# Kernel optimization log

Measured on AMD Instinct MI355X. Metric: run time of the kernel, lower is better.

The kernel has to match this reference:

```python
import jax, jax.numpy as jnp
import numpy as np

DEPTH = 16
Q_DIM = 64
V_DIM = 64
BATCH = 2048


def setup_inputs() -> dict:
    key = jax.random.key(0)
    k1, k2, k3 = jax.random.split(key, 3)
    query = jax.random.normal(k1, (BATCH, Q_DIM), dtype=jnp.float32)
    # internal-node keys: (2^depth - 1) nodes, each with 2 child keys of dim q_dim
    tree_key = jax.random.normal(k2, (2 ** DEPTH - 1, 2, Q_DIM), dtype=jnp.float32)
    # leaf values: 2^depth leaves of dim v_dim
    tree_value = jax.random.normal(k3, (2 ** DEPTH, V_DIM), dtype=jnp.float32)
    return {"query": query, "tree_key": tree_key, "tree_value": tree_value}


def _tree_attention(query, tree_key, tree_value, depth):
    # Hierarchical softmax attention over a complete binary tree.
    # At each internal node, a 2-way softmax over <query, child_key> logits
    # splits probability mass between left/right subtrees; leaf weight is the
    # product of probabilities along its root-to-leaf path.
    B = query.shape[0]
    probs = jnp.ones((B, 1), dtype=query.dtype)
    start = 0
    for d in range(depth):
        n = 2 ** d  # nodes at this level, stored contiguously at [start, start+n)
        level_keys = tree_key[start:start + n]           # (n, 2, q_dim)
        logits = jnp.einsum('bq,ncq->bnc', query, level_keys)  # (B, n, 2)
        p = jax.nn.softmax(logits, axis=-1)               # (B, n, 2)
        probs = (probs[:, :, None] * p).reshape(B, 2 * n)  # (B, 2n)
        start += n
    # weighted combination of leaf values: (B, 2^depth) @ (2^depth, v_dim)
    return probs @ tree_value


def reference(query, tree_key, tree_value):
    return _tree_attention(query, tree_key, tree_value, DEPTH)
```

## Files before the change

### kernel.cpp

```cpp
#include <hip/hip_runtime.h>

#define LOG2E 1.44269504088896f

typedef _Float16 half8  __attribute__((ext_vector_type(8)));
typedef _Float16 half4v __attribute__((ext_vector_type(4)));
typedef float    floatx4 __attribute__((ext_vector_type(4)));

#define WS_KD   0u
#define WS_VT   8388608u
#define WS_PART 16777216u

__device__ __forceinline__ floatx4 mfma16(half8 a, half8 b, floatx4 c) {
    return __builtin_amdgcn_mfma_f32_16x16x32_f16(a, b, c, 0, 0, 0);
}

__device__ __forceinline__ float sigmf(float d) {
    return __builtin_amdgcn_rcpf(1.0f + __builtin_amdgcn_exp2f(d * (-LOG2E)));
}

__device__ __forceinline__ void wave_lds_fence() {
    asm volatile("s_waitcnt lgkmcnt(0)" ::: "memory");
    __builtin_amdgcn_sched_barrier(0);
}

__global__ __launch_bounds__(256)
void k_prep(const float* __restrict__ tkey, const float* __restrict__ tval,
            char* __restrict__ ws)
{
    __shared__ _Float16 sT[64 * 72];
    const int bid = blockIdx.x, tid = threadIdx.x;

    {
        const int l = tid >> 2, part = tid & 3;
        const floatx4* vp = (const floatx4*)(tval + ((size_t)bid * 64 + l) * 64) + part * 4;
        #pragma unroll
        for (int t4 = 0; t4 < 4; ++t4) {
            floatx4 f = vp[t4];
            #pragma unroll
            for (int e = 0; e < 4; ++e)
                sT[(part * 16 + t4 * 4 + e) * 72 + l] = (_Float16)f[e];
        }
    }
    __syncthreads();
    {
        const int v = tid >> 2, q4 = tid & 3;
        half8 x0 = *(const half8*)(sT + v * 72 + 16 * q4);
        half8 x1 = *(const half8*)(sT + v * 72 + 16 * q4 + 8);
        char* base = ws + WS_VT + (size_t)bid * 8192;
        const int nt = v >> 4, lmv = v & 15;
        const int u0 = 2 * q4, u1 = 2 * q4 + 1;
        *(half8*)(base + (nt * 2 + (u0 >> 2)) * 1024 + (((u0 & 3) << 4) | lmv) * 16) = x0;
        *(half8*)(base + (nt * 2 + (u1 >> 2)) * 1024 + (((u1 & 3) << 4) | lmv) * 16) = x1;
    }

    #pragma unroll
    for (int k = 0; k < 2; ++k) {
        const int gt  = bid * 512 + k * 256 + tid;
        const int rid = gt >> 3, part = gt & 7;
        const int s = rid >> 6, j = rid & 63;
        const size_t dst = (size_t)WS_KD + (size_t)s * 8192
                         + ((j >> 4) * 2 + (part >> 2)) * 1024
                         + (((part & 3) << 4) | (j & 15)) * 16;
        half8 out;
        if (j < 63) {
            const int u = j + 1;
            const int f = 31 - __builtin_clz(u);
            const int i = u - (1 << f);
            const int gidx = ((1 << (10 + f)) - 1) + (s << f) + i;
            const floatx4* kp = (const floatx4*)(tkey + (size_t)gidx * 128) + part * 2;
            floatx4 a0 = kp[0], a1 = kp[1];
            floatx4 b0 = kp[16], b1 = kp[17];
            #pragma unroll
            for (int e = 0; e < 4; ++e) {
                out[e]     = (_Float16)(a0[e] - b0[e]);
                out[4 + e] = (_Float16)(a1[e] - b1[e]);
            }
        } else {
            #pragma unroll
            for (int e = 0; e < 8; ++e) out[e] = (_Float16)0.f;
        }
        *(half8*)(ws + dst) = out;
    }
}

__global__ __launch_bounds__(256, 2)
void k_main(const float* __restrict__ q,
            const float* __restrict__ tkey,
            const char* __restrict__ wsc,
            _Float16* __restrict__ pout)
{
    __shared__ _Float16 sW[4 * 64 * 72];

    const int tid  = threadIdx.x;
    const int w    = tid >> 6;
    const int lane = tid & 63;
    const int lm   = lane & 15;
    const int quad = lane >> 4;
    const int xcd  = blockIdx.x & 7;
    const int ix   = blockIdx.x >> 3;
    const int g    = xcd * 8 + (ix >> 3);
    const int tb   = ix & 7;

    _Float16* R = sW + w * (64 * 72);

    half8 qA[4][2];
    #pragma unroll
    for (int m = 0; m < 4; ++m)
        #pragma unroll
        for (int kt = 0; kt < 2; ++kt) {
            const int row = tb * 256 + 64 * w + 16 * m + lm;
            const floatx4* qp = (const floatx4*)(q + (size_t)row * 64 + kt * 32 + quad * 8);
            floatx4 f0 = qp[0], f1 = qp[1];
            half8 hv;
            #pragma unroll
            for (int e = 0; e < 4; ++e) { hv[e] = (_Float16)f0[e]; hv[4 + e] = (_Float16)f1[e]; }
            qA[m][kt] = hv;
        }

    half8 pbf[2][2];
    #pragma unroll
    for (int nt = 0; nt < 2; ++nt) {
        const int j = 16 * nt + lm;
        int gidx = -1;
        if (j < 6) {
            gidx = (1 << j) - 1 + (g >> (6 - j));
        } else if (j < 21) {
            const int u = j - 5;
            const int e = 31 - __builtin_clz(u);
            const int i = u - (1 << e);
            gidx = ((1 << (6 + e)) - 1) + (g << e) + i;
        }
        #pragma unroll
        for (int kt = 0; kt < 2; ++kt) {
            half8 out;
            if (gidx >= 0) {
                const floatx4* kp = (const floatx4*)(tkey + (size_t)gidx * 128 + kt * 32 + quad * 8);
                floatx4 a0 = kp[0], a1 = kp[1];
                floatx4 b0 = kp[16], b1 = kp[17];
                #pragma unroll
                for (int e = 0; e < 4; ++e) {
                    out[e]     = (_Float16)(a0[e] - b0[e]);
                    out[4 + e] = (_Float16)(a1[e] - b1[e]);
                }
            } else {
                #pragma unroll
                for (int e = 0; e < 8; ++e) out[e] = (_Float16)0.f;
            }
            pbf[nt][kt] = out;
        }
    }

    #pragma unroll
    for (int nt = 0; nt < 2; ++nt) {
        floatx4 acc[4];
        #pragma unroll
        for (int m = 0; m < 4; ++m) {
            acc[m][0] = 0.f; acc[m][1] = 0.f; acc[m][2] = 0.f; acc[m][3] = 0.f;
            acc[m] = mfma16(pbf[nt][0], qA[m][0], acc[m]);
            acc[m] = mfma16(pbf[nt][1], qA[m][1], acc[m]);
        }
        #pragma unroll
        for (int m = 0; m < 4; ++m) {
            half4v ph;
            #pragma unroll
            for (int r = 0; r < 4; ++r) ph[r] = (_Float16)sigmf(acc[m][r]);
            *(half4v*)(R + (16 * m + lm) * 72 + 16 * nt + 4 * quad) = ph;
        }
    }
    wave_lds_fence();

    float pref = 1.f;
    #pragma unroll
    for (int d = 0; d < 6; ++d) {
        float pv = (float)R[lane * 72 + d];
        pref *= ((g >> (5 - d)) & 1) ? (1.f - pv) : pv;
    }
    const float p6    = (float)R[lane * 72 + 6];
    const float p7_0  = (float)R[lane * 72 + 7],  p7_1  = (float)R[lane * 72 + 8];
    const float p9_0  = (float)R[lane * 72 + 9],  p9_1  = (float)R[lane * 72 + 10];
    const float p9_2  = (float)R[lane * 72 + 11], p9_3  = (float)R[lane * 72 + 12];
    const float p13_0 = (float)R[lane * 72 + 13], p13_1 = (float)R[lane * 72 + 14];
    const float p13_2 = (float)R[lane * 72 + 15], p13_3 = (float)R[lane * 72 + 16];
    const float p13_4 = (float)R[lane * 72 + 17], p13_5 = (float)R[lane * 72 + 18];
    const float p13_6 = (float)R[lane * 72 + 19], p13_7 = (float)R[lane * 72 + 20];
    wave_lds_fence();

    floatx4 O[4][4];
    #pragma unroll
    for (int m = 0; m < 4; ++m)
        #pragma unroll
        for (int nt = 0; nt < 4; ++nt) { O[m][nt][0]=0.f; O[m][nt][1]=0.f; O[m][nt][2]=0.f; O[m][nt][3]=0.f; }

    for (int sl = 0; sl < 16; ++sl) {
        const int s = (g << 4) + sl;

        const char* kdp = wsc + WS_KD + (size_t)s * 8192;
        const char* vtp = wsc + WS_VT + (size_t)s * 8192;
        half8 bfr[4][2], vf[4][2];
        #pragma unroll
        for (int nt = 0; nt < 4; ++nt)
            #pragma unroll
            for (int kt = 0; kt < 2; ++kt) {
                bfr[nt][kt] = *(const half8*)(kdp + (nt * 2 + kt) * 1024 + lane * 16);
                vf[nt][kt]  = *(const half8*)(vtp + (nt * 2 + kt) * 1024 + lane * 16);
            }

        __builtin_amdgcn_s_setprio(1);
        #pragma unroll
        for (int nt = 0; nt < 4; ++nt) {
            floatx4 acc[4];
            #pragma unroll
            for (int m = 0; m < 4; ++m) {
                acc[m][0] = 0.f; acc[m][1] = 0.f; acc[m][2] = 0.f; acc[m][3] = 0.f;
                acc[m] = mfma16(bfr[nt][0], qA[m][0], acc[m]);
                acc[m] = mfma16(bfr[nt][1], qA[m][1], acc[m]);
            }
            #pragma unroll
            for (int m = 0; m < 4; ++m) {
                half4v ph;
                #pragma unroll
                for (int r = 0; r < 4; ++r) ph[r] = (_Float16)sigmf(acc[m][r]);
                *(half4v*)(R + (16 * m + lm) * 72 + 16 * nt + 4 * quad) = ph;
            }
        }
        __builtin_amdgcn_s_setprio(0);
        wave_lds_fence();

        const int a0 = sl >> 3, a1 = sl >> 2, a2 = sl >> 1;
        float P0v = pref * (a0 ? (1.f - p6) : p6);
        { float v7 = a0 ? p7_1 : p7_0;                    P0v *= (a1 & 1) ? (1.f - v7) : v7; }
        { float v9 = (a1 == 0) ? p9_0 : (a1 == 1) ? p9_1 : (a1 == 2) ? p9_2 : p9_3;
                                                          P0v *= (a2 & 1) ? (1.f - v9) : v9; }
        { float vd = (a2 == 0) ? p13_0 : (a2 == 1) ? p13_1 : (a2 == 2) ? p13_2 : (a2 == 3) ? p13_3
                   : (a2 == 4) ? p13_4 : (a2 == 5) ? p13_5 : (a2 == 6) ? p13_6 : p13_7;
                                                          P0v *= (sl & 1) ? (1.f - vd) : vd; }

        half8 pr[8];
        #pragma unroll
        for (int t = 0; t < 8; ++t)
            pr[t] = *(const half8*)(R + lane * 72 + t * 8);
        #define PN(n) ((float)pr[(n) >> 3][(n) & 7])

        #pragma unroll
        for (int qq = 0; qq < 4; ++qq) {
            float p0 = PN(0);
            float p1 = PN(1 + (qq >> 1));
            float P2 = P0v * (((qq >> 1) & 1) ? (1.f - p0) : p0)
                           * ((qq & 1) ? (1.f - p1) : p1);
            float p2 = PN(3 + qq);
            float A3[2]; A3[0] = P2 * p2; A3[1] = P2 * (1.f - p2);
            float A4[4];
            #pragma unroll
            for (int c = 0; c < 2; ++c) {
                float pv = PN(7 + 2 * qq + c);
                A4[2 * c] = A3[c] * pv; A4[2 * c + 1] = A3[c] * (1.f - pv);
            }
            float A5[8];
            #pragma unroll
            for (int n = 0; n < 4; ++n) {
                float pv = PN(15 + 4 * qq + n);
                A5[2 * n] = A4[n] * pv; A5[2 * n + 1] = A4[n] * (1.f - pv);
            }
            half8 lo, hi;
            #pragma unroll
            for (int n = 0; n < 8; ++n) {
                float pv = PN(31 + 8 * qq + n);
                float e0 = A5[n] * pv;
                float e1 = A5[n] * (1.f - pv);
                if (n < 4) { lo[2 * n] = (_Float16)e0; lo[2 * n + 1] = (_Float16)e1; }
                else       { hi[2 * (n - 4)] = (_Float16)e0; hi[2 * (n - 4) + 1] = (_Float16)e1; }
            }
            const int sw = (lane & 7) << 3;
            *(half8*)(R + lane * 72 + ((16 * qq)     ^ sw)) = lo;
            *(half8*)(R + lane * 72 + ((16 * qq + 8) ^ sw)) = hi;
        }
        #undef PN
        wave_lds_fence();

        {
            half8 af[4][2];
            #pragma unroll
            for (int m = 0; m < 4; ++m) {
                const int rA = 16 * m + lm;
                const int sw = (lm & 7) << 3;
                #pragma unroll
                for (int kt = 0; kt < 2; ++kt)
                    af[m][kt] = *(const half8*)(R + rA * 72 + ((kt * 32 + quad * 8) ^ sw));
            }
            __builtin_amdgcn_s_setprio(1);
            #pragma unroll
            for (int nt = 0; nt < 4; ++nt)
                #pragma unroll
                for (int kt = 0; kt < 2; ++kt) {
                    O[0][nt] = mfma16(af[0][kt], vf[nt][kt], O[0][nt]);
                    O[1][nt] = mfma16(af[1][kt], vf[nt][kt], O[1][nt]);
                    O[2][nt] = mfma16(af[2][kt], vf[nt][kt], O[2][nt]);
                    O[3][nt] = mfma16(af[3][kt], vf[nt][kt], O[3][nt]);
                }
            __builtin_amdgcn_s_setprio(0);
        }
    }

    wave_lds_fence();
    #pragma unroll
    for (int m = 0; m < 4; ++m)
        #pragma unroll
        for (int nt = 0; nt < 4; ++nt)
            #pragma unroll
            for (int r = 0; r < 4; ++r) {
                const int row = 16 * m + 4 * quad + r;
                const int col = 16 * nt + lm;
                R[row * 72 + (col ^ ((row & 7) << 3))] = (_Float16)O[m][nt][r];
            }
    wave_lds_fence();
    {
        _Float16* dst = pout + ((size_t)g * 2048 + tb * 256 + 64 * w + lane) * 64;
        const int sw = (lane & 7) << 3;
        #pragma unroll
        for (int j = 0; j < 8; ++j)
            *(half8*)(dst + j * 8) = *(const half8*)(R + lane * 72 + ((j * 8) ^ sw));
    }
}

__global__ __launch_bounds__(256)
void k_reduce(const _Float16* __restrict__ part, float* __restrict__ outp)
{
    const int idx = blockIdx.x * 256 + threadIdx.x;
    float s0 = 0.f, s1 = 0.f, s2 = 0.f, s3 = 0.f;
    #pragma unroll 8
    for (int gg = 0; gg < 64; ++gg) {
        half4v v = *(const half4v*)(part + (size_t)gg * 131072 + (size_t)idx * 4);
        s0 += (float)v[0]; s1 += (float)v[1]; s2 += (float)v[2]; s3 += (float)v[3];
    }
    floatx4 o; o[0] = s0; o[1] = s1; o[2] = s2; o[3] = s3;
    *(floatx4*)(outp + (size_t)idx * 4) = o;
}

extern "C" void kernel_launch(void* const* d_in, const int* in_sizes, int n_in,
                              void* d_out, int out_size, void* d_ws, size_t ws_size,
                              hipStream_t stream)
{
    const float* q  = (const float*)d_in[0];
    const float* tk = (const float*)d_in[1];
    const float* tv = (const float*)d_in[2];
    float* outp = (float*)d_out;
    char*  ws   = (char*)d_ws;
    _Float16* partp = (_Float16*)(ws + WS_PART);

    k_prep  <<<dim3(1024), dim3(256), 0, stream>>>(tk, tv, ws);
    k_main  <<<dim3(512),  dim3(256), 0, stream>>>(q, tk, ws, partp);
    k_reduce<<<dim3(128),  dim3(256), 0, stream>>>(partp, outp);
}
```

Baseline: 167.8 us.

## Halve rows per wave and split leaf expansion across half-waves

```diff
diff --git a/kernel.cpp b/kernel.cpp
--- a/kernel.cpp
+++ b/kernel.cpp
@@ -61,23 +61,21 @@
         const size_t dst = (size_t)WS_KD + (size_t)s * 8192
                          + ((j >> 4) * 2 + (part >> 2)) * 1024
                          + (((part & 3) << 4) | (j & 15)) * 16;
+        const int h = j >> 5, loc = j & 31;
+        int u;
+        if (loc == 0) u = 1;
+        else { const int e = 31 - __builtin_clz(loc); u = loc + (1 << e) * (1 + h); }
+        const int f = 31 - __builtin_clz(u);
+        const int i = u - (1 << f);
+        const int gidx = ((1 << (10 + f)) - 1) + (s << f) + i;
+        const floatx4* kp = (const floatx4*)(tkey + (size_t)gidx * 128) + part * 2;
+        floatx4 a0 = kp[0], a1 = kp[1];
+        floatx4 b0 = kp[16], b1 = kp[17];
         half8 out;
-        if (j < 63) {
-            const int u = j + 1;
-            const int f = 31 - __builtin_clz(u);
-            const int i = u - (1 << f);
-            const int gidx = ((1 << (10 + f)) - 1) + (s << f) + i;
-            const floatx4* kp = (const floatx4*)(tkey + (size_t)gidx * 128) + part * 2;
-            floatx4 a0 = kp[0], a1 = kp[1];
-            floatx4 b0 = kp[16], b1 = kp[17];
-            #pragma unroll
-            for (int e = 0; e < 4; ++e) {
-                out[e]     = (_Float16)(a0[e] - b0[e]);
-                out[4 + e] = (_Float16)(a1[e] - b1[e]);
-            }
-        } else {
-            #pragma unroll
-            for (int e = 0; e < 8; ++e) out[e] = (_Float16)0.f;
+        #pragma unroll
+        for (int e = 0; e < 4; ++e) {
+            out[e]     = (_Float16)(a0[e] - b0[e]);
+            out[4 + e] = (_Float16)(a1[e] - b1[e]);
         }
         *(half8*)(ws + dst) = out;
     }
@@ -89,26 +87,29 @@
             const char* __restrict__ wsc,
             _Float16* __restrict__ pout)
 {
-    __shared__ _Float16 sW[4 * 64 * 72];
+    __shared__ _Float16 sW[4 * (32 * 72 + 32 * 64)];
 
     const int tid  = threadIdx.x;
     const int w    = tid >> 6;
     const int lane = tid & 63;
     const int lm   = lane & 15;
     const int quad = lane >> 4;
+    const int h    = lane >> 5;
+    const int bb   = lane & 31;
     const int xcd  = blockIdx.x & 7;
     const int ix   = blockIdx.x >> 3;
-    const int g    = xcd * 8 + (ix >> 3);
-    const int tb   = ix & 7;
-
-    _Float16* R = sW + w * (64 * 72);
-
-    half8 qA[4][2];
-    #pragma unroll
-    for (int m = 0; m < 4; ++m)
+    const int g    = xcd * 8 + (ix >> 4);
+    const int tb   = ix & 15;
+
+    _Float16* Rn = sW + w * (32 * 72 + 32 * 64);
+    _Float16* Rl = Rn + 32 * 72;
+
+    half8 qA[2][2];
+    #pragma unroll
+    for (int m = 0; m < 2; ++m)
         #pragma unroll
         for (int kt = 0; kt < 2; ++kt) {
-            const int row = tb * 256 + 64 * w + 16 * m + lm;
+            const int row = tb * 128 + 32 * w + 16 * m + lm;
             const floatx4* qp = (const floatx4*)(q + (size_t)row * 64 + kt * 32 + quad * 8);
             floatx4 f0 = qp[0], f1 = qp[1];
             half8 hv;
@@ -152,19 +153,19 @@
 
     #pragma unroll
     for (int nt = 0; nt < 2; ++nt) {
-        floatx4 acc[4];
-        #pragma unroll
-        for (int m = 0; m < 4; ++m) {
+        floatx4 acc[2];
+        #pragma unroll
+        for (int m = 0; m < 2; ++m) {
             acc[m][0] = 0.f; acc[m][1] = 0.f; acc[m][2] = 0.f; acc[m][3] = 0.f;
             acc[m] = mfma16(pbf[nt][0], qA[m][0], acc[m]);
             acc[m] = mfma16(pbf[nt][1], qA[m][1], acc[m]);
         }
         #pragma unroll
-        for (int m = 0; m < 4; ++m) {
+        for (int m = 0; m < 2; ++m) {
             half4v ph;
             #pragma unroll
             for (int r = 0; r < 4; ++r) ph[r] = (_Float16)sigmf(acc[m][r]);
-            *(half4v*)(R + (16 * m + lm) * 72 + 16 * nt + 4 * quad) = ph;
+            *(half4v*)(Rn + (16 * m + lm) * 72 + 16 * nt + 4 * quad) = ph;
         }
     }
     wave_lds_fence();
@@ -172,22 +173,22 @@
     float pref = 1.f;
     #pragma unroll
     for (int d = 0; d < 6; ++d) {
-        float pv = (float)R[lane * 72 + d];
+        float pv = (float)Rn[bb * 72 + d];
         pref *= ((g >> (5 - d)) & 1) ? (1.f - pv) : pv;
     }
-    const float p6    = (float)R[lane * 72 + 6];
-    const float p7_0  = (float)R[lane * 72 + 7],  p7_1  = (float)R[lane * 72 + 8];
-    const float p9_0  = (float)R[lane * 72 + 9],  p9_1  = (float)R[lane * 72 + 10];
-    const float p9_2  = (float)R[lane * 72 + 11], p9_3  = (float)R[lane * 72 + 12];
-    const float p13_0 = (float)R[lane * 72 + 13], p13_1 = (float)R[lane * 72 + 14];
-    const float p13_2 = (float)R[lane * 72 + 15], p13_3 = (float)R[lane * 72 + 16];
-    const float p13_4 = (float)R[lane * 72 + 17], p13_5 = (float)R[lane * 72 + 18];
-    const float p13_6 = (float)R[lane * 72 + 19], p13_7 = (float)R[lane * 72 + 20];
+    const float p6    = (float)Rn[bb * 72 + 6];
+    const float p7_0  = (float)Rn[bb * 72 + 7],  p7_1  = (float)Rn[bb * 72 + 8];
+    const float p9_0  = (float)Rn[bb * 72 + 9],  p9_1  = (float)Rn[bb * 72 + 10];
+    const float p9_2  = (float)Rn[bb * 72 + 11], p9_3  = (float)Rn[bb * 72 + 12];
+    const float p13_0 = (float)Rn[bb * 72 + 13], p13_1 = (float)Rn[bb * 72 + 14];
+    const float p13_2 = (float)Rn[bb * 72 + 15], p13_3 = (float)Rn[bb * 72 + 16];
+    const float p13_4 = (float)Rn[bb * 72 + 17], p13_5 = (float)Rn[bb * 72 + 18];
+    const float p13_6 = (float)Rn[bb * 72 + 19], p13_7 = (float)Rn[bb * 72 + 20];
     wave_lds_fence();
 
-    floatx4 O[4][4];
-    #pragma unroll
-    for (int m = 0; m < 4; ++m)
+    floatx4 O[2][4];
+    #pragma unroll
+    for (int m = 0; m < 2; ++m)
         #pragma unroll
         for (int nt = 0; nt < 4; ++nt) { O[m][nt][0]=0.f; O[m][nt][1]=0.f; O[m][nt][2]=0.f; O[m][nt][3]=0.f; }
 
@@ -208,19 +209,19 @@
         __builtin_amdgcn_s_setprio(1);
         #pragma unroll
         for (int nt = 0; nt < 4; ++nt) {
-            floatx4 acc[4];
-            #pragma unroll
-            for (int m = 0; m < 4; ++m) {
+            floatx4 acc[2];
+            #pragma unroll
+            for (int m = 0; m < 2; ++m) {
                 acc[m][0] = 0.f; acc[m][1] = 0.f; acc[m][2] = 0.f; acc[m][3] = 0.f;
                 acc[m] = mfma16(bfr[nt][0], qA[m][0], acc[m]);
                 acc[m] = mfma16(bfr[nt][1], qA[m][1], acc[m]);
             }
             #pragma unroll
-            for (int m = 0; m < 4; ++m) {
+            for (int m = 0; m < 2; ++m) {
                 half4v ph;
                 #pragma unroll
                 for (int r = 0; r < 4; ++r) ph[r] = (_Float16)sigmf(acc[m][r]);
-                *(half4v*)(R + (16 * m + lm) * 72 + 16 * nt + 4 * quad) = ph;
+                *(half4v*)(Rn + (16 * m + lm) * 72 + 16 * nt + 4 * quad) = ph;
             }
         }
         __builtin_amdgcn_s_setprio(0);
@@ -235,57 +236,59 @@
                    : (a2 == 4) ? p13_4 : (a2 == 5) ? p13_5 : (a2 == 6) ? p13_6 : p13_7;
                                                           P0v *= (sl & 1) ? (1.f - vd) : vd; }
 
-        half8 pr[8];
-        #pragma unroll
-        for (int t = 0; t < 8; ++t)
-            pr[t] = *(const half8*)(R + lane * 72 + t * 8);
-        #define PN(n) ((float)pr[(n) >> 3][(n) & 7])
-
-        #pragma unroll
-        for (int qq = 0; qq < 4; ++qq) {
-            float p0 = PN(0);
-            float p1 = PN(1 + (qq >> 1));
-            float P2 = P0v * (((qq >> 1) & 1) ? (1.f - p0) : p0)
-                           * ((qq & 1) ? (1.f - p1) : p1);
-            float p2 = PN(3 + qq);
-            float A3[2]; A3[0] = P2 * p2; A3[1] = P2 * (1.f - p2);
-            float A4[4];
-            #pragma unroll
-            for (int c = 0; c < 2; ++c) {
-                float pv = PN(7 + 2 * qq + c);
-                A4[2 * c] = A3[c] * pv; A4[2 * c + 1] = A3[c] * (1.f - pv);
-            }
-            float A5[8];
-            #pragma unroll
-            for (int n = 0; n < 4; ++n) {
-                float pv = PN(15 + 4 * qq + n);
-                A5[2 * n] = A4[n] * pv; A5[2 * n + 1] = A4[n] * (1.f - pv);
-            }
-            half8 lo, hi;
-            #pragma unroll
-            for (int n = 0; n < 8; ++n) {
-                float pv = PN(31 + 8 * qq + n);
-                float e0 = A5[n] * pv;
-                float e1 = A5[n] * (1.f - pv);
-                if (n < 4) { lo[2 * n] = (_Float16)e0; lo[2 * n + 1] = (_Float16)e1; }
-                else       { hi[2 * (n - 4)] = (_Float16)e0; hi[2 * (n - 4) + 1] = (_Float16)e1; }
-            }
-            const int sw = (lane & 7) << 3;
-            *(half8*)(R + lane * 72 + ((16 * qq)     ^ sw)) = lo;
-            *(half8*)(R + lane * 72 + ((16 * qq + 8) ^ sw)) = hi;
-        }
-        #undef PN
+        half8 pr4[4];
+        #pragma unroll
+        for (int t = 0; t < 4; ++t)
+            pr4[t] = *(const half8*)(Rn + bb * 72 + 32 * h + t * 8);
+        #define PN4(n) ((float)pr4[(n) >> 3][(n) & 7])
+
+        {
+            float p0 = PN4(0), p1 = PN4(1);
+            const float base = P0v * (h ? (1.f - p0) : p0);
+            #pragma unroll
+            for (int ql = 0; ql < 2; ++ql) {
+                float P2 = base * (ql ? (1.f - p1) : p1);
+                float p2 = PN4(2 + ql);
+                float A3[2]; A3[0] = P2 * p2; A3[1] = P2 * (1.f - p2);
+                float A4[4];
+                #pragma unroll
+                for (int c = 0; c < 2; ++c) {
+                    float pv = PN4(4 + 2 * ql + c);
+                    A4[2 * c] = A3[c] * pv; A4[2 * c + 1] = A3[c] * (1.f - pv);
+                }
+                float A5[8];
+                #pragma unroll
+                for (int n = 0; n < 4; ++n) {
+                    float pv = PN4(8 + 4 * ql + n);
+                    A5[2 * n] = A4[n] * pv; A5[2 * n + 1] = A4[n] * (1.f - pv);
+                }
+                half8 lo, hi;
+                #pragma unroll
+                for (int n = 0; n < 8; ++n) {
+                    float pv = PN4(16 + 8 * ql + n);
+                    float e0 = A5[n] * pv;
+                    float e1 = A5[n] * (1.f - pv);
+                    if (n < 4) { lo[2 * n] = (_Float16)e0; lo[2 * n + 1] = (_Float16)e1; }
+                    else       { hi[2 * (n - 4)] = (_Float16)e0; hi[2 * (n - 4) + 1] = (_Float16)e1; }
+                }
+                const int sw = (bb & 7) << 3;
+                const int cb = 32 * h + 16 * ql;
+                *(half8*)(Rl + bb * 64 + (cb ^ sw))       = lo;
+                *(half8*)(Rl + bb * 64 + ((cb + 8) ^ sw)) = hi;
+            }
+        }
+        #undef PN4
         wave_lds_fence();
 
         {
-            half8 af[4][2];
-            #pragma unroll
-            for (int m = 0; m < 4; ++m) {
+            half8 af[2][2];
+            #pragma unroll
+            for (int m = 0; m < 2; ++m) {
                 const int rA = 16 * m + lm;
                 const int sw = (lm & 7) << 3;
                 #pragma unroll
                 for (int kt = 0; kt < 2; ++kt)
-                    af[m][kt] = *(const half8*)(R + rA * 72 + ((kt * 32 + quad * 8) ^ sw));
+                    af[m][kt] = *(const half8*)(Rl + rA * 64 + ((kt * 32 + quad * 8) ^ sw));
             }
             __builtin_amdgcn_s_setprio(1);
             #pragma unroll
@@ -294,8 +297,6 @@
                 for (int kt = 0; kt < 2; ++kt) {
                     O[0][nt] = mfma16(af[0][kt], vf[nt][kt], O[0][nt]);
                     O[1][nt] = mfma16(af[1][kt], vf[nt][kt], O[1][nt]);
-                    O[2][nt] = mfma16(af[2][kt], vf[nt][kt], O[2][nt]);
-                    O[3][nt] = mfma16(af[3][kt], vf[nt][kt], O[3][nt]);
                 }
             __builtin_amdgcn_s_setprio(0);
         }
@@ -303,22 +304,22 @@
 
     wave_lds_fence();
     #pragma unroll
-    for (int m = 0; m < 4; ++m)
+    for (int m = 0; m < 2; ++m)
         #pragma unroll
         for (int nt = 0; nt < 4; ++nt)
             #pragma unroll
             for (int r = 0; r < 4; ++r) {
                 const int row = 16 * m + 4 * quad + r;
                 const int col = 16 * nt + lm;
-                R[row * 72 + (col ^ ((row & 7) << 3))] = (_Float16)O[m][nt][r];
+                Rl[row * 64 + (col ^ ((row & 7) << 3))] = (_Float16)O[m][nt][r];
             }
     wave_lds_fence();
     {
-        _Float16* dst = pout + ((size_t)g * 2048 + tb * 256 + 64 * w + lane) * 64;
-        const int sw = (lane & 7) << 3;
-        #pragma unroll
-        for (int j = 0; j < 8; ++j)
-            *(half8*)(dst + j * 8) = *(const half8*)(R + lane * 72 + ((j * 8) ^ sw));
+        _Float16* dst = pout + ((size_t)g * 2048 + tb * 128 + 32 * w + bb) * 64 + 32 * h;
+        const int sw = (bb & 7) << 3;
+        #pragma unroll
+        for (int j = 0; j < 4; ++j)
+            *(half8*)(dst + j * 8) = *(const half8*)(Rl + bb * 64 + ((32 * h + j * 8) ^ sw));
     }
 }
 
@@ -348,6 +349,6 @@
     _Float16* partp = (_Float16*)(ws + WS_PART);
 
     k_prep  <<<dim3(1024), dim3(256), 0, stream>>>(tk, tv, ws);
-    k_main  <<<dim3(512),  dim3(256), 0, stream>>>(q, tk, ws, partp);
+    k_main  <<<dim3(1024), dim3(256), 0, stream>>>(q, tk, ws, partp);
     k_reduce<<<dim3(128),  dim3(256), 0, stream>>>(partp, outp);
 }
```

New measurement: 168.7 us. Within noise of the previous version (+0.5%).
